# Kernel optimization log

Hardware: AMD Instinct MI355X
Metric: run time of the kernel (lower is better)

## Reference

```python
import jax, jax.numpy as jnp
import numpy as np

DIM = 2048
NUM_HEADS = 32
NUM_KV_HEADS = 8
HEAD_DIM = DIM // NUM_HEADS            # 64
NUM_GROUPS = NUM_HEADS // NUM_KV_HEADS  # 4
ROPE_THETA = 10000.0
BATCH = 2
SEQ = 2048


def _rope_cos_sin(seq_len, head_dim, theta, dtype):
    # rope_percentage = 1.0 -> rotary applied to full head_dim
    inv_freq = 1.0 / (theta ** (jnp.arange(0, head_dim, 2, dtype=jnp.float32) / head_dim))
    pos = jnp.arange(seq_len, dtype=jnp.float32)
    freqs = pos[:, None] * inv_freq[None, :]          # [S, hd/2]
    emb = jnp.concatenate([freqs, freqs], axis=-1)    # [S, hd]
    return jnp.cos(emb).astype(dtype), jnp.sin(emb).astype(dtype)


def _rotate_half(t):
    half = t.shape[-1] // 2
    return jnp.concatenate([-t[..., half:], t[..., :half]], axis=-1)


def _apply_rope(t, cos, sin):
    # t: [B, H, S, hd]; cos/sin: [S, hd]
    return t * cos[None, None, :, :] + _rotate_half(t) * sin[None, None, :, :]


def setup_inputs() -> dict:
    key = jax.random.key(0)
    kx, kq, kk, kv, ko = jax.random.split(key, 5)
    scale = 0.02
    return {
        "x": jax.random.normal(kx, (BATCH, SEQ, DIM), dtype=jnp.float32),
        "Wq": jax.random.normal(kq, (DIM, NUM_HEADS * HEAD_DIM), dtype=jnp.float32) * scale,
        "Wk": jax.random.normal(kk, (DIM, NUM_KV_HEADS * HEAD_DIM), dtype=jnp.float32) * scale,
        "Wv": jax.random.normal(kv, (DIM, NUM_KV_HEADS * HEAD_DIM), dtype=jnp.float32) * scale,
        "Wo": jax.random.normal(ko, (NUM_HEADS * HEAD_DIM, DIM), dtype=jnp.float32) * scale,
    }


def reference(x, Wq, Wk, Wv, Wo):
    B, S, D = x.shape
    # projections (use_bias=False)
    q = (x @ Wq).reshape(B, S, NUM_HEADS, HEAD_DIM).transpose(0, 2, 1, 3)     # [B,H,S,hd]
    k = (x @ Wk).reshape(B, S, NUM_KV_HEADS, HEAD_DIM).transpose(0, 2, 1, 3)  # [B,KV,S,hd]
    v = (x @ Wv).reshape(B, S, NUM_KV_HEADS, HEAD_DIM).transpose(0, 2, 1, 3)  # [B,KV,S,hd]

    cos, sin = _rope_cos_sin(S, HEAD_DIM, ROPE_THETA, x.dtype)
    q = _apply_rope(q, cos, sin)
    k = _apply_rope(k, cos, sin)

    # grouped KV broadcast: each kv head serves NUM_GROUPS query heads
    k = jnp.repeat(k, NUM_GROUPS, axis=1)  # [B,H,S,hd]
    v = jnp.repeat(v, NUM_GROUPS, axis=1)  # [B,H,S,hd]

    scale = 1.0 / jnp.sqrt(jnp.asarray(HEAD_DIM, dtype=x.dtype))
    scores = jnp.einsum('bhqd,bhkd->bhqk', q, k) * scale  # [B,H,S,S]
    weights = jax.nn.softmax(scores, axis=-1)             # dropout_rate=0 -> no-op
    attn = jnp.einsum('bhqk,bhkd->bhqd', weights, v)      # [B,H,S,hd]

    attn = attn.transpose(0, 2, 1, 3).reshape(B, S, NUM_HEADS * HEAD_DIM)
    return attn @ Wo                                      # [B,S,D]
```

## Files before the change

### kernel.cpp

```cpp
#include <hip/hip_runtime.h>

#define B_   2
#define S_   2048
#define D_   2048
#define H_   32
#define KV_  8
#define HD_  64
#define TOK_ (B_*S_)
#define NQKV_ 3072

typedef __attribute__((ext_vector_type(8))) short short8;
typedef __attribute__((ext_vector_type(4))) float f32x4;
typedef __attribute__((ext_vector_type(16))) float f32x16;

#define OFF_XB   ((size_t)0)
#define OFF_WQKV (OFF_XB   + (size_t)TOK_*D_*2)
#define OFF_WO   (OFF_WQKV + (size_t)NQKV_*D_*2)
#define OFF_QKV  (OFF_WO   + (size_t)D_*D_*2)
#define OFF_VT   (OFF_QKV  + (size_t)TOK_*NQKV_*2)
#define OFF_AO   (OFF_VT   + (size_t)B_*KV_*HD_*S_*2)
#define OFF_TAB  (OFF_AO   + (size_t)TOK_*D_*2)

__device__ __forceinline__ unsigned short f2bfu(float f) {
  unsigned int x = __float_as_uint(f);
  x += 0x7fffu + ((x >> 16) & 1u);
  return (unsigned short)(x >> 16);
}
__device__ __forceinline__ float bf2f(unsigned short u) {
  return __uint_as_float(((unsigned int)u) << 16);
}
__device__ __forceinline__ unsigned int pk2(float a, float b) {
  return (unsigned int)f2bfu(a) | ((unsigned int)f2bfu(b) << 16);
}
__device__ __forceinline__ void gld16(const void* g, void* l) {
  __builtin_amdgcn_global_load_lds((const __attribute__((address_space(1))) void*)g,
                                   (__attribute__((address_space(3))) void*)l, 16, 0, 0);
}

__global__ __launch_bounds__(256) void ropetab_k(float2* tab) {
  int i = blockIdx.x * 256 + threadIdx.x;
  int s = i >> 5, j = i & 31;
  float inv = exp2f(-(float)j * (13.287712379549449f / 32.0f));
  float ang = (float)s * inv;
  tab[i] = make_float2(cosf(ang), sinf(ang));
}

__global__ __launch_bounds__(256) void cvtx_k(const float4* __restrict__ x, ushort4* __restrict__ xb) {
  int i = blockIdx.x * 256 + threadIdx.x;
  float4 f = x[i];
  ushort4 o;
  o.x = f2bfu(f.x); o.y = f2bfu(f.y); o.z = f2bfu(f.z); o.w = f2bfu(f.w);
  xb[i] = o;
}

__global__ __launch_bounds__(256) void wtrans_k(const float* __restrict__ in, unsigned short* __restrict__ out, int N) {
  __shared__ float tile[32][33];
  int n0 = blockIdx.x * 32, k0 = blockIdx.y * 32;
  int tx = threadIdx.x, ty = threadIdx.y;
#pragma unroll
  for (int i = 0; i < 4; ++i)
    tile[ty + 8*i][tx] = in[(size_t)(k0 + ty + 8*i) * N + n0 + tx];
  __syncthreads();
#pragma unroll
  for (int i = 0; i < 4; ++i)
    out[(size_t)(n0 + ty + 8*i) * 2048 + k0 + tx] = f2bfu(tile[tx][ty + 8*i]);
}

template<int OUTF32>
__global__ __launch_bounds__(256) void gemm_bt(const unsigned short* __restrict__ A,
                                               const unsigned short* __restrict__ Bt,
                                               void* __restrict__ Cout, int M, int N, int K) {
  __shared__ unsigned short Al[2][128][32];
  __shared__ unsigned short Bl[2][128][32];
  int tid = threadIdx.x, lane = tid & 63, w = tid >> 6;
  int lr = lane & 15, lg = lane >> 4;
  int wr = w >> 1, wc = w & 1;
  int m0 = blockIdx.y * 128, n0 = blockIdx.x * 128;
  int trow = tid >> 2, tseg = tid & 3;

  auto stage = [&](int buf, int kt) {
    gld16(A + (size_t)(m0 + trow) * K + kt * 32 + tseg * 8, &Al[buf][trow][tseg * 8]);
    gld16(A + (size_t)(m0 + 64 + trow) * K + kt * 32 + tseg * 8, &Al[buf][64 + trow][tseg * 8]);
    gld16(Bt + (size_t)(n0 + trow) * K + kt * 32 + tseg * 8, &Bl[buf][trow][tseg * 8]);
    gld16(Bt + (size_t)(n0 + 64 + trow) * K + kt * 32 + tseg * 8, &Bl[buf][64 + trow][tseg * 8]);
  };

  f32x4 zero4 = {0.f, 0.f, 0.f, 0.f};
  f32x4 acc[4][4];
#pragma unroll
  for (int mi = 0; mi < 4; ++mi)
#pragma unroll
    for (int ni = 0; ni < 4; ++ni) acc[mi][ni] = zero4;

  int nk = K >> 5;
  stage(0, 0);
  int buf = 0;
  for (int kt = 0; kt < nk; ++kt) {
    __syncthreads();
    if (kt + 1 < nk) stage(buf ^ 1, kt + 1);
    short8 af[4], bfr[4];
#pragma unroll
    for (int i = 0; i < 4; ++i) {
      af[i]  = *(const short8*)&Al[buf][64 * wr + 16 * i + lr][lg * 8];
      bfr[i] = *(const short8*)&Bl[buf][64 * wc + 16 * i + lr][lg * 8];
    }
#pragma unroll
    for (int mi = 0; mi < 4; ++mi)
#pragma unroll
      for (int ni = 0; ni < 4; ++ni)
        acc[mi][ni] = __builtin_amdgcn_mfma_f32_16x16x32_bf16(af[mi], bfr[ni], acc[mi][ni], 0, 0, 0);
    buf ^= 1;
  }
#pragma unroll
  for (int mi = 0; mi < 4; ++mi)
#pragma unroll
    for (int ni = 0; ni < 4; ++ni)
#pragma unroll
      for (int r = 0; r < 4; ++r) {
        int row = m0 + 64 * wr + 16 * mi + lg * 4 + r;
        int col = n0 + 64 * wc + 16 * ni + lr;
        float v = acc[mi][ni][r];
        if (OUTF32) ((float*)Cout)[(size_t)row * N + col] = v;
        else ((unsigned short*)Cout)[(size_t)row * N + col] = f2bfu(v);
      }
}

__global__ __launch_bounds__(256) void rope_k(unsigned short* __restrict__ qkv, const float2* __restrict__ tab) {
  int idx = blockIdx.x * 256 + threadIdx.x;
  int tok = idx / 1280, r = idx % 1280;
  int col, j;
  if (r < 1024) { j = r & 31; col = (r >> 5) * 64 + j; }
  else { int rr = r - 1024; j = rr & 31; col = 2048 + (rr >> 5) * 64 + j; }
  int s = tok & (S_ - 1);
  float2 cs = tab[s * 32 + j];
  unsigned short* p = qkv + (size_t)tok * NQKV_ + col;
  float a = bf2f(p[0]), b = bf2f(p[32]);
  p[0]  = f2bfu(a * cs.x - b * cs.y);
  p[32] = f2bfu(b * cs.x + a * cs.y);
}

__global__ __launch_bounds__(256) void vtrans_k(const unsigned short* __restrict__ qkv, unsigned short* __restrict__ vt) {
  __shared__ unsigned short tile[32][33];
  int s0 = blockIdx.x * 32;
  int y0 = blockIdx.y * 32;
  int bkv = y0 >> 6, d0 = y0 & 63;
  int b = bkv >> 3, kv = bkv & 7;
  int tx = threadIdx.x, ty = threadIdx.y;
#pragma unroll
  for (int i = 0; i < 4; ++i)
    tile[ty + 8*i][tx] = qkv[(size_t)(b * S_ + s0 + ty + 8*i) * NQKV_ + 2560 + kv * 64 + d0 + tx];
  __syncthreads();
#pragma unroll
  for (int i = 0; i < 4; ++i)
    vt[(size_t)(y0 + ty + 8*i) * (size_t)S_ + s0 + tx] = tile[tx][ty + 8*i];
}

#define RLOG 0.1803368801111179f
#define THRRAW 44.0f
__global__ __launch_bounds__(256, 4) void attn_k(const unsigned short* __restrict__ qkv,
                                                 const unsigned short* __restrict__ vt,
                                                 unsigned short* __restrict__ ao) {
  __shared__ unsigned short Kl[2][64][64];
  __shared__ unsigned short Vl[2][64][64];
  int bh = blockIdx.x, b = bh >> 5, h = bh & 31, kvh = h >> 2;
  int q0 = blockIdx.y * 128;
  int tid = threadIdx.x, w = tid >> 6, lane = tid & 63;
  int lq = lane & 31, hf = lane >> 5;
  int swk = lq & 7;

  const unsigned short* qp = qkv + (size_t)(b * S_ + q0 + w * 32 + lq) * NQKV_ + h * 64 + hf * 8;
  short8 qf[4];
#pragma unroll
  for (int k = 0; k < 4; ++k) qf[k] = *(const short8*)(qp + k * 16);

  const unsigned short* kbase = qkv + (size_t)(b * S_) * NQKV_ + 2048 + kvh * 64;
  const unsigned short* vbase = vt + (size_t)(b * KV_ + kvh) * 64 * S_;
  int srow = tid >> 3, sslot = tid & 7;
  int scol = (sslot ^ (srow & 7)) * 8;

  auto stageKV = [&](int buf, int kv0) {
#pragma unroll
    for (int sh = 0; sh < 2; ++sh) {
      gld16(kbase + (size_t)(kv0 + 32 * sh + srow) * NQKV_ + scol, &Kl[buf][32 * sh + srow][sslot * 8]);
      gld16(vbase + (size_t)(32 * sh + srow) * S_ + kv0 + scol, &Vl[buf][32 * sh + srow][sslot * 8]);
    }
  };

  f32x16 O0, O1;
#pragma unroll
  for (int r = 0; r < 16; ++r) { O0[r] = 0.f; O1[r] = 0.f; }
  float rmax = -1e30f, rsum = 0.f;

  stageKV(0, 0);
  int buf = 0;
  for (int it = 0; it < S_ / 64; ++it) {
    __syncthreads();
    if (it + 1 < S_ / 64) stageKV(buf ^ 1, (it + 1) * 64);

    f32x16 sa, sb;
#pragma unroll
    for (int r = 0; r < 16; ++r) { sa[r] = 0.f; sb[r] = 0.f; }
#pragma unroll
    for (int kst = 0; kst < 4; ++kst) {
      short8 kf = *(const short8*)&Kl[buf][lq][((kst * 2 + hf) ^ swk) * 8];
      sa = __builtin_amdgcn_mfma_f32_32x32x16_bf16(kf, qf[kst], sa, 0, 0, 0);
    }
#pragma unroll
    for (int kst = 0; kst < 4; ++kst) {
      short8 kf = *(const short8*)&Kl[buf][32 + lq][((kst * 2 + hf) ^ swk) * 8];
      sb = __builtin_amdgcn_mfma_f32_32x32x16_bf16(kf, qf[kst], sb, 0, 0, 0);
    }

    float pm = sa[0];
#pragma unroll
    for (int r = 1; r < 16; ++r) pm = fmaxf(pm, sa[r]);
#pragma unroll
    for (int r = 0; r < 16; ++r) pm = fmaxf(pm, sb[r]);
    pm = fmaxf(pm, __shfl_xor(pm, 32));

    if (!__all(pm - rmax <= THRRAW)) {
      float mn = fmaxf(rmax, pm);
      float corr = exp2f((rmax - mn) * RLOG);
      rmax = mn;
      rsum *= corr;
      float co[16];
#pragma unroll
      for (int r = 0; r < 16; ++r) co[r] = __shfl(corr, (r & 3) + 8 * (r >> 2) + 4 * hf);
#pragma unroll
      for (int r = 0; r < 16; ++r) { O0[r] *= co[r]; O1[r] *= co[r]; }
    }

    float mk = rmax * RLOG;
    float rs = 0.f;
#pragma unroll
    for (int r = 0; r < 16; ++r) { float p = exp2f(sa[r] * RLOG - mk); sa[r] = p; rs += p; }
#pragma unroll
    for (int r = 0; r < 16; ++r) { float p = exp2f(sb[r] * RLOG - mk); sb[r] = p; rs += p; }
    rs += __shfl_xor(rs, 32);
    rsum += rs;

    auto pv_sub = [&](const f32x16& sc, int ks) {
#pragma unroll
      for (int k16 = 0; k16 < 2; ++k16) {
        unsigned int c01 = pk2(sc[k16 * 8 + 0], sc[k16 * 8 + 1]);
        unsigned int c23 = pk2(sc[k16 * 8 + 2], sc[k16 * 8 + 3]);
        unsigned int c45 = pk2(sc[k16 * 8 + 4], sc[k16 * 8 + 5]);
        unsigned int c67 = pk2(sc[k16 * 8 + 6], sc[k16 * 8 + 7]);
        unsigned int x01 = __shfl_xor(c01, 32);
        unsigned int x23 = __shfl_xor(c23, 32);
        unsigned int x45 = __shfl_xor(c45, 32);
        unsigned int x67 = __shfl_xor(c67, 32);
        union { unsigned int u[4]; short8 s8; } pu;
        pu.u[0] = hf ? x45 : c01;
        pu.u[1] = hf ? x67 : c23;
        pu.u[2] = hf ? c45 : x01;
        pu.u[3] = hf ? c67 : x23;
        int kk = ks * 2 + k16;
        short8 v0 = *(const short8*)&Vl[buf][lq][((kk * 2 + hf) ^ swk) * 8];
        O0 = __builtin_amdgcn_mfma_f32_32x32x16_bf16(pu.s8, v0, O0, 0, 0, 0);
        short8 v1 = *(const short8*)&Vl[buf][32 + lq][((kk * 2 + hf) ^ swk) * 8];
        O1 = __builtin_amdgcn_mfma_f32_32x32x16_bf16(pu.s8, v1, O1, 0, 0, 0);
      }
    };
    pv_sub(sa, 0);
    pv_sub(sb, 1);
    buf ^= 1;
  }

  float inv = 1.f / rsum;
#pragma unroll
  for (int r = 0; r < 16; ++r) {
    int qr = (r & 3) + 8 * (r >> 2) + 4 * hf;
    float io = __shfl(inv, qr);
    size_t row = (size_t)(b * S_ + q0 + w * 32 + qr);
    ao[row * D_ + h * 64 + lq]      = f2bfu(O0[r] * io);
    ao[row * D_ + h * 64 + 32 + lq] = f2bfu(O1[r] * io);
  }
}

extern "C" void kernel_launch(void* const* d_in, const int* in_sizes, int n_in,
                              void* d_out, int out_size, void* d_ws, size_t ws_size,
                              hipStream_t stream) {
  const float* x  = (const float*)d_in[0];
  const float* Wq = (const float*)d_in[1];
  const float* Wk = (const float*)d_in[2];
  const float* Wv = (const float*)d_in[3];
  const float* Wo = (const float*)d_in[4];

  char* ws = (char*)d_ws;
  unsigned short* xb    = (unsigned short*)(ws + OFF_XB);
  unsigned short* wqkvt = (unsigned short*)(ws + OFF_WQKV);
  unsigned short* wot   = (unsigned short*)(ws + OFF_WO);
  unsigned short* qkv   = (unsigned short*)(ws + OFF_QKV);
  unsigned short* vt    = (unsigned short*)(ws + OFF_VT);
  unsigned short* ao    = (unsigned short*)(ws + OFF_AO);
  float2*         tab   = (float2*)(ws + OFF_TAB);

  ropetab_k<<<dim3(256), dim3(256), 0, stream>>>(tab);
  cvtx_k<<<dim3((TOK_*D_/4)/256), dim3(256), 0, stream>>>((const float4*)x, (ushort4*)xb);
  wtrans_k<<<dim3(64, 64), dim3(32, 8), 0, stream>>>(Wq, wqkvt, 2048);
  wtrans_k<<<dim3(16, 64), dim3(32, 8), 0, stream>>>(Wk, wqkvt + (size_t)2048 * 2048, 512);
  wtrans_k<<<dim3(16, 64), dim3(32, 8), 0, stream>>>(Wv, wqkvt + (size_t)2560 * 2048, 512);
  wtrans_k<<<dim3(64, 64), dim3(32, 8), 0, stream>>>(Wo, wot, 2048);

  gemm_bt<0><<<dim3(NQKV_/128, TOK_/128), dim3(256), 0, stream>>>(xb, wqkvt, (void*)qkv, TOK_, NQKV_, D_);
  rope_k<<<dim3(TOK_ * 1280 / 256), dim3(256), 0, stream>>>(qkv, tab);
  vtrans_k<<<dim3(S_/32, (B_*KV_*HD_)/32), dim3(32, 8), 0, stream>>>(qkv, vt);
  attn_k<<<dim3(B_*H_, S_/128), dim3(256), 0, stream>>>(qkv, vt, ao);
  gemm_bt<1><<<dim3(D_/128, TOK_/128), dim3(256), 0, stream>>>(ao, wot, d_out, TOK_, D_, D_);
}
```

Before: 292.4 us.

## Load K/V fragments straight from global into registers in attention, remap workgroups per XCD

Removes the LDS double-buffered K/V staging and barriers from the attention kernel; each lane now loads its K and V MFMA fragments directly from global memory into registers every iteration. It also remaps workgroup IDs so that blocks sharing a batch-head land on the same XCD, which should improve L2 reuse of K/V. The row-max reduction becomes a tree, and bf16 packing switches to the HIP intrinsic. The trade-off is that each wave now redundantly fetches K/V with strided, uncoalesced global loads and has no software prefetch overlap, relying on caches and occupancy instead.

```diff
diff --git a/kernel.cpp b/kernel.cpp
--- a/kernel.cpp
+++ b/kernel.cpp
@@ -1,4 +1,5 @@
 #include <hip/hip_runtime.h>
+#include <hip/hip_bf16.h>
 
 #define B_   2
 #define S_   2048
@@ -30,7 +31,9 @@
   return __uint_as_float(((unsigned int)u) << 16);
 }
 __device__ __forceinline__ unsigned int pk2(float a, float b) {
-  return (unsigned int)f2bfu(a) | ((unsigned int)f2bfu(b) << 16);
+  union { __hip_bfloat162 h; unsigned int u; } t;
+  t.h = __float22bfloat162_rn(make_float2(a, b));
+  return t.u;
 }
 __device__ __forceinline__ void gld16(const void* g, void* l) {
   __builtin_amdgcn_global_load_lds((const __attribute__((address_space(1))) void*)g,
@@ -157,16 +160,17 @@
 
 #define RLOG 0.1803368801111179f
 #define THRRAW 44.0f
-__global__ __launch_bounds__(256, 4) void attn_k(const unsigned short* __restrict__ qkv,
-                                                 const unsigned short* __restrict__ vt,
-                                                 unsigned short* __restrict__ ao) {
-  __shared__ unsigned short Kl[2][64][64];
-  __shared__ unsigned short Vl[2][64][64];
-  int bh = blockIdx.x, b = bh >> 5, h = bh & 31, kvh = h >> 2;
-  int q0 = blockIdx.y * 128;
+__global__ __launch_bounds__(256) void attn_k(const unsigned short* __restrict__ qkv,
+                                              const unsigned short* __restrict__ vt,
+                                              unsigned short* __restrict__ ao) {
+  int wgid = blockIdx.x + 64 * blockIdx.y;
+  int xcd = wgid & 7, c = wgid >> 3;
+  int bh = xcd * 8 + (c & 7);
+  int qt = c >> 3;
+  int b = bh >> 5, h = bh & 31, kvh = h >> 2;
+  int q0 = qt * 128;
   int tid = threadIdx.x, w = tid >> 6, lane = tid & 63;
   int lq = lane & 31, hf = lane >> 5;
-  int swk = lq & 7;
 
   const unsigned short* qp = qkv + (size_t)(b * S_ + q0 + w * 32 + lq) * NQKV_ + h * 64 + hf * 8;
   short8 qf[4];
@@ -175,48 +179,50 @@
 
   const unsigned short* kbase = qkv + (size_t)(b * S_) * NQKV_ + 2048 + kvh * 64;
   const unsigned short* vbase = vt + (size_t)(b * KV_ + kvh) * 64 * S_;
-  int srow = tid >> 3, sslot = tid & 7;
-  int scol = (sslot ^ (srow & 7)) * 8;
-
-  auto stageKV = [&](int buf, int kv0) {
-#pragma unroll
-    for (int sh = 0; sh < 2; ++sh) {
-      gld16(kbase + (size_t)(kv0 + 32 * sh + srow) * NQKV_ + scol, &Kl[buf][32 * sh + srow][sslot * 8]);
-      gld16(vbase + (size_t)(32 * sh + srow) * S_ + kv0 + scol, &Vl[buf][32 * sh + srow][sslot * 8]);
-    }
-  };
+  const unsigned short* kR0 = kbase + (size_t)lq * NQKV_ + hf * 8;
+  const unsigned short* kR1 = kbase + (size_t)(32 + lq) * NQKV_ + hf * 8;
+  const unsigned short* vR0 = vbase + (size_t)lq * S_ + hf * 8;
+  const unsigned short* vR1 = vbase + (size_t)(32 + lq) * S_ + hf * 8;
 
   f32x16 O0, O1;
 #pragma unroll
   for (int r = 0; r < 16; ++r) { O0[r] = 0.f; O1[r] = 0.f; }
   float rmax = -1e30f, rsum = 0.f;
 
-  stageKV(0, 0);
-  int buf = 0;
   for (int it = 0; it < S_ / 64; ++it) {
-    __syncthreads();
-    if (it + 1 < S_ / 64) stageKV(buf ^ 1, (it + 1) * 64);
+    size_t koff = (size_t)(it * 64) * NQKV_;
+    int voff = it * 64;
+
+    short8 ka[4], kb[4], va[4], vb[4];
+#pragma unroll
+    for (int kst = 0; kst < 4; ++kst) {
+      ka[kst] = *(const short8*)(kR0 + koff + kst * 16);
+      kb[kst] = *(const short8*)(kR1 + koff + kst * 16);
+    }
+#pragma unroll
+    for (int kk = 0; kk < 4; ++kk) {
+      va[kk] = *(const short8*)(vR0 + voff + kk * 16);
+      vb[kk] = *(const short8*)(vR1 + voff + kk * 16);
+    }
 
     f32x16 sa, sb;
 #pragma unroll
     for (int r = 0; r < 16; ++r) { sa[r] = 0.f; sb[r] = 0.f; }
 #pragma unroll
-    for (int kst = 0; kst < 4; ++kst) {
-      short8 kf = *(const short8*)&Kl[buf][lq][((kst * 2 + hf) ^ swk) * 8];
-      sa = __builtin_amdgcn_mfma_f32_32x32x16_bf16(kf, qf[kst], sa, 0, 0, 0);
-    }
-#pragma unroll
-    for (int kst = 0; kst < 4; ++kst) {
-      short8 kf = *(const short8*)&Kl[buf][32 + lq][((kst * 2 + hf) ^ swk) * 8];
-      sb = __builtin_amdgcn_mfma_f32_32x32x16_bf16(kf, qf[kst], sb, 0, 0, 0);
-    }
-
-    float pm = sa[0];
-#pragma unroll
-    for (int r = 1; r < 16; ++r) pm = fmaxf(pm, sa[r]);
-#pragma unroll
-    for (int r = 0; r < 16; ++r) pm = fmaxf(pm, sb[r]);
-    pm = fmaxf(pm, __shfl_xor(pm, 32));
+    for (int kst = 0; kst < 4; ++kst)
+      sa = __builtin_amdgcn_mfma_f32_32x32x16_bf16(ka[kst], qf[kst], sa, 0, 0, 0);
+#pragma unroll
+    for (int kst = 0; kst < 4; ++kst)
+      sb = __builtin_amdgcn_mfma_f32_32x32x16_bf16(kb[kst], qf[kst], sb, 0, 0, 0);
+
+    float mx[16];
+#pragma unroll
+    for (int r = 0; r < 16; ++r) mx[r] = fmaxf(sa[r], sb[r]);
+#pragma unroll
+    for (int s = 8; s >= 1; s >>= 1)
+#pragma unroll
+      for (int r = 0; r < s; ++r) mx[r] = fmaxf(mx[r], mx[r + s]);
+    float pm = fmaxf(mx[0], __shfl_xor(mx[0], 32));
 
     if (!__all(pm - rmax <= THRRAW)) {
       float mn = fmaxf(rmax, pm);
@@ -256,15 +262,12 @@
         pu.u[2] = hf ? c45 : x01;
         pu.u[3] = hf ? c67 : x23;
         int kk = ks * 2 + k16;
-        short8 v0 = *(const short8*)&Vl[buf][lq][((kk * 2 + hf) ^ swk) * 8];
-        O0 = __builtin_amdgcn_mfma_f32_32x32x16_bf16(pu.s8, v0, O0, 0, 0, 0);
-        short8 v1 = *(const short8*)&Vl[buf][32 + lq][((kk * 2 + hf) ^ swk) * 8];
-        O1 = __builtin_amdgcn_mfma_f32_32x32x16_bf16(pu.s8, v1, O1, 0, 0, 0);
+        O0 = __builtin_amdgcn_mfma_f32_32x32x16_bf16(pu.s8, va[kk], O0, 0, 0, 0);
+        O1 = __builtin_amdgcn_mfma_f32_32x32x16_bf16(pu.s8, vb[kk], O1, 0, 0, 0);
       }
     };
     pv_sub(sa, 0);
     pv_sub(sb, 1);
-    buf ^= 1;
   }
 
   float inv = 1.f / rsum;
@@ -306,6 +309,6 @@
   gemm_bt<0><<<dim3(NQKV_/128, TOK_/128), dim3(256), 0, stream>>>(xb, wqkvt, (void*)qkv, TOK_, NQKV_, D_);
   rope_k<<<dim3(TOK_ * 1280 / 256), dim3(256), 0, stream>>>(qkv, tab);
   vtrans_k<<<dim3(S_/32, (B_*KV_*HD_)/32), dim3(32, 8), 0, stream>>>(qkv, vt);
-  attn_k<<<dim3(B_*H_, S_/128), dim3(256), 0, stream>>>(qkv, vt, ao);
+  attn_k<<<dim3(64, 16), dim3(256), 0, stream>>>(qkv, vt, ao);
   gemm_bt<1><<<dim3(D_/128, TOK_/128), dim3(256), 0, stream>>>(ao, wot, d_out, TOK_, D_, D_);
 }
```

Result: slower. 396.2 us (+35.5%).
